# Kernel optimization log

Measured on AMD Instinct MI355X. Metric: run time of the kernel, lower is better.

## Reference

```python
import jax, jax.numpy as jnp
import numpy as np

K = 512
D = 256


def setup_inputs() -> dict:
    key = jax.random.key(0)
    k1, k2 = jax.random.split(key)
    z_e = jax.random.normal(k1, (64, D, 32, 32), dtype=jnp.float32)
    # torch init: uniform_(-1/K, 1/K)
    codebook = jax.random.uniform(k2, (K, D), dtype=jnp.float32, minval=-1.0 / K, maxval=1.0 / K)
    return {"z_e": z_e, "codebook": codebook}


def reference(z_e, codebook):
    B, C, H, W = z_e.shape
    # (B,C,H,W) -> (B,H,W,C) -> (N,D)
    z_flat = jnp.transpose(z_e, (0, 2, 3, 1)).reshape(-1, C)
    # squared L2 distances: ||z||^2 + ||e||^2 - 2 z.e  -> [N, K]
    d = (jnp.sum(z_flat ** 2, axis=1, keepdims=True)
         + jnp.sum(codebook ** 2, axis=1)
         - 2.0 * jnp.matmul(z_flat, codebook.T))
    idx = jnp.argmin(d, axis=1)  # [N]
    z_q_flat = codebook[idx]  # [N, D] gather
    z_q = jnp.transpose(z_q_flat.reshape(B, H, W, C), (0, 3, 1, 2))
    commitment_loss = jnp.mean((z_e - jax.lax.stop_gradient(z_q)) ** 2)
    codebook_loss = jnp.mean((z_q - jax.lax.stop_gradient(z_e)) ** 2)
    # straight-through estimator
    z_q_st = z_e + jax.lax.stop_gradient(z_q - z_e)
    indices = idx.reshape(B, H, W)
    return (z_q_st, commitment_loss, codebook_loss, indices)
```

## Files before the change

### kernel.cpp

```cpp
#include <hip/hip_runtime.h>


typedef __attribute__((ext_vector_type(8))) short short8v;
typedef __attribute__((ext_vector_type(4))) float float4v;
typedef unsigned short ushort_t;

namespace {
constexpr int K = 512;
constexpr int D = 256;
constexpr int HW = 1024;
constexpr int NROWS = 65536;
constexpr int CHW = D * HW;

constexpr int ZQ_SIZE = 64 * CHW;
constexpr int LOSS0_OFF = ZQ_SIZE;
constexpr int LOSS1_OFF = ZQ_SIZE + 1;
constexpr int IDX_OFF = ZQ_SIZE + 2;

constexpr int WS_EH_FLOATS = (K * D) / 2;
constexpr int WS_B = WS_EH_FLOATS;
constexpr int WS_PART = WS_B + K;
constexpr int NBLK = NROWS / 32;

constexpr float EPS_CAND = 2.5e-3f;
}

__device__ __forceinline__ ushort_t bf16_rne(float f) {
    unsigned u = __float_as_uint(f);
    u += 0x7fffu + ((u >> 16) & 1u);
    return (ushort_t)(u >> 16);
}
__device__ __forceinline__ float bf16_to_f(ushort_t h) {
    return __uint_as_float((unsigned)h << 16);
}

__global__ void vq_prep(const float* __restrict__ cb, float* __restrict__ ws) {
    const int k = blockIdx.x;
    const int t = threadIdx.x;
    ushort_t* eh = (ushort_t*)ws;
    eh[(size_t)k * D + t] = bf16_rne(cb[k * D + t]);
    __shared__ float r16[16];
    if (t < 16) {
#pragma clang fp contract(off)
        const float* x = cb + k * D + (t >> 3) * 128;
        const int j = t & 7;
        float v = x[j];
        float r = v * v;
        for (int i = 1; i < 16; ++i) {
            float w = x[8 * i + j];
            r += w * w;
        }
        r16[t] = r;
    }
    __syncthreads();
    if (t == 0) {
#pragma clang fp contract(off)
        float lo = ((r16[0] + r16[1]) + (r16[2] + r16[3])) +
                   ((r16[4] + r16[5]) + (r16[6] + r16[7]));
        float hi = ((r16[8] + r16[9]) + (r16[10] + r16[11])) +
                   ((r16[12] + r16[13]) + (r16[14] + r16[15]));
        ws[WS_B + k] = lo + hi;
    }
}

__global__ __launch_bounds__(256, 2) void vq_mega(
    const float* __restrict__ z_e, const float* __restrict__ cb,
    const ushort_t* __restrict__ eh, const float* __restrict__ Bv,
    float* __restrict__ part, float* __restrict__ out) {
    __shared__ float zf[D][32];
    __shared__ __align__(16) ushort_t zh[32][264];
    __shared__ __align__(16) ushort_t zl[32][264];
    __shared__ float lds_B[K];
    __shared__ float lds_scratch[32][16];
    __shared__ float lds_A[32];
    __shared__ float wmin[4][32];
    __shared__ float rmin[32];
    __shared__ int cnt[32];
    __shared__ float wpart[4];

    const int t = threadIdx.x;
    const int row0 = blockIdx.x * 32;
    const int b = row0 >> 10;
    const int hw0 = row0 & 1023;

    {
        const float4* zb4 = reinterpret_cast<const float4*>(z_e + (size_t)b * CHW + hw0);
        float4* lz4 = reinterpret_cast<float4*>(&zf[0][0]);
        for (int i = t; i < 2048; i += 256) {
            int c = i >> 3, j4 = i & 7;
            lz4[c * 8 + j4] = zb4[c * 256 + j4];
        }
        lds_B[t] = Bv[t];
        lds_B[t + 256] = Bv[t + 256];
    }
    __syncthreads();

    {
#pragma clang fp contract(off)
        const int row = t >> 3;
        const int half = (t >> 2) & 1;
        const int j0 = (t & 3) * 2;
        const int cbase = half * 128;
        float v0 = zf[cbase + j0][row];
        float v1 = zf[cbase + j0 + 1][row];
        float r0 = v0 * v0;
        float r1 = v1 * v1;
        for (int i = 1; i < 16; ++i) {
            float w0 = zf[cbase + 8 * i + j0][row];
            float w1 = zf[cbase + 8 * i + j0 + 1][row];
            r0 += w0 * w0;
            r1 += w1 * w1;
        }
        lds_scratch[row][half * 8 + j0] = r0;
        lds_scratch[row][half * 8 + j0 + 1] = r1;
    }
    {
        const int row = t & 31;
        const int dc = t >> 5;
#pragma unroll
        for (int i = 0; i < 8; ++i) {
            const int d4 = dc * 32 + i * 4;
            ushort_t h[4], l[4];
#pragma unroll
            for (int q = 0; q < 4; ++q) {
                float f = zf[d4 + q][row];
                h[q] = bf16_rne(f);
                l[q] = bf16_rne(f - bf16_to_f(h[q]));
            }
            uint2 ph, pl;
            ph.x = (unsigned)h[0] | ((unsigned)h[1] << 16);
            ph.y = (unsigned)h[2] | ((unsigned)h[3] << 16);
            pl.x = (unsigned)l[0] | ((unsigned)l[1] << 16);
            pl.y = (unsigned)l[2] | ((unsigned)l[3] << 16);
            *reinterpret_cast<uint2*>(&zh[row][d4]) = ph;
            *reinterpret_cast<uint2*>(&zl[row][d4]) = pl;
        }
    }
    __syncthreads();
    if (t < 32) {
#pragma clang fp contract(off)
        const float* r = lds_scratch[t];
        float lo = ((r[0] + r[1]) + (r[2] + r[3])) + ((r[4] + r[5]) + (r[6] + r[7]));
        float hi = ((r[8] + r[9]) + (r[10] + r[11])) + ((r[12] + r[13]) + (r[14] + r[15]));
        lds_A[t] = lo + hi;
    }
    __syncthreads();

    const int lane = t & 63;
    const int w = t >> 6;
    const int wc0 = w * 128;
    const int l15 = lane & 15;
    const int kg = lane >> 4;

    float4v acc[8][2];
#pragma unroll
    for (int c = 0; c < 8; ++c)
#pragma unroll
        for (int rt = 0; rt < 2; ++rt) acc[c][rt] = (float4v)0.f;

    const ushort_t* ehp = eh + (size_t)(wc0 + l15) * D + 8 * kg;

#pragma unroll 4
    for (int d0 = 0; d0 < D; d0 += 32) {
        const short8v bh0 = *reinterpret_cast<const short8v*>(&zh[l15][d0 + 8 * kg]);
        const short8v bh1 = *reinterpret_cast<const short8v*>(&zh[16 + l15][d0 + 8 * kg]);
        const short8v bl0 = *reinterpret_cast<const short8v*>(&zl[l15][d0 + 8 * kg]);
        const short8v bl1 = *reinterpret_cast<const short8v*>(&zl[16 + l15][d0 + 8 * kg]);
#pragma unroll
        for (int c = 0; c < 8; ++c) {
            const short8v a = *reinterpret_cast<const short8v*>(ehp + c * 16 * D + d0);
            acc[c][0] = __builtin_amdgcn_mfma_f32_16x16x32_bf16(a, bh0, acc[c][0], 0, 0, 0);
            acc[c][1] = __builtin_amdgcn_mfma_f32_16x16x32_bf16(a, bh1, acc[c][1], 0, 0, 0);
            acc[c][0] = __builtin_amdgcn_mfma_f32_16x16x32_bf16(a, bl0, acc[c][0], 0, 0, 0);
            acc[c][1] = __builtin_amdgcn_mfma_f32_16x16x32_bf16(a, bl1, acc[c][1], 0, 0, 0);
        }
    }

    float lmin0 = 3.0e38f, lmin1 = 3.0e38f;
#pragma unroll
    for (int c = 0; c < 8; ++c)
#pragma unroll
        for (int rt = 0; rt < 2; ++rt)
#pragma unroll
            for (int r = 0; r < 4; ++r) {
                const int code = wc0 + 16 * c + 4 * kg + r;
                const int row = rt * 16 + l15;
                float s = (lds_A[row] + lds_B[code]) - 2.0f * acc[c][rt][r];
                acc[c][rt][r] = s;
                if (rt == 0) lmin0 = fminf(lmin0, s);
                else lmin1 = fminf(lmin1, s);
            }
    lmin0 = fminf(lmin0, __shfl_xor(lmin0, 16));
    lmin0 = fminf(lmin0, __shfl_xor(lmin0, 32));
    lmin1 = fminf(lmin1, __shfl_xor(lmin1, 16));
    lmin1 = fminf(lmin1, __shfl_xor(lmin1, 32));
    if (lane < 16) {
        wmin[w][l15] = lmin0;
        wmin[w][16 + l15] = lmin1;
    }
    __syncthreads();
    if (t < 32) {
        rmin[t] = fminf(fminf(wmin[0][t], wmin[1][t]), fminf(wmin[2][t], wmin[3][t]));
        cnt[t] = 0;
    }
    __syncthreads();

    int* cand = reinterpret_cast<int*>(&lds_scratch[0][0]);
#pragma unroll
    for (int c = 0; c < 8; ++c)
#pragma unroll
        for (int rt = 0; rt < 2; ++rt) {
            const int row = rt * 16 + l15;
            const float thr = rmin[row] + EPS_CAND;
#pragma unroll
            for (int r = 0; r < 4; ++r) {
                if (acc[c][rt][r] <= thr) {
                    const int code = wc0 + 16 * c + 4 * kg + r;
                    int slot = atomicAdd(&cnt[row], 1);
                    if (slot < 15) cand[row * 15 + slot] = code;
                }
            }
        }
    __syncthreads();

    float* ed = reinterpret_cast<float*>(&zh[0][0]);
    int* ek = reinterpret_cast<int*>(ed + 256);
    int* kb = ek + 256;
    {
        const int row = t & 31;
        const int ct = t >> 5;
        int n = cnt[row];
        if (n > 15) n = 15;
        float bd = 3.0e38f;
        int bk = 0x7fffffff;
        if (n == 1) {
            if (ct == 0) {
                bd = -3.0e38f;
                bk = cand[row * 15];
            }
        } else {
            for (int s = ct; s < n; s += 8) {
                const int k = cand[row * 15 + s];
                const float* ep = cb + (size_t)k * D;
                float a = 0.f;
#pragma unroll 8
                for (int c = 0; c < D; ++c) a = fmaf(zf[c][row], ep[c], a);
                float dv;
                {
#pragma clang fp contract(off)
                    float t1 = lds_A[row] + lds_B[k];
                    dv = t1 - 2.0f * a;
                }
                if (dv < bd || (dv == bd && k < bk)) {
                    bd = dv;
                    bk = k;
                }
            }
        }
        ed[t] = bd;
        ek[t] = bk;
    }
    __syncthreads();
    if (t < 32) {
        float bd = ed[t];
        int bk = ek[t];
#pragma unroll
        for (int q = 1; q < 8; ++q) {
            float od = ed[q * 32 + t];
            int ok = ek[q * 32 + t];
            if (od < bd || (od == bd && ok < bk)) {
                bd = od;
                bk = ok;
            }
        }
        kb[t] = bk;
        out[IDX_OFF + row0 + t] = (float)bk;
    }
    __syncthreads();

    {
        const int j = t & 31;
        const int g = t >> 5;
        const int kme = kb[j];
        const float* ep = cb + (size_t)kme * D;
        float* ob = out + (size_t)b * CHW + hw0;
        float accum = 0.f;
#pragma unroll 4
        for (int i = 0; i < 32; ++i) {
            const int c = g * 32 + i;
            float z = zf[c][j];
            float e = ep[c];
            ob[c * HW + j] = z + (e - z);
            float df = z - e;
            accum = fmaf(df, df, accum);
        }
#pragma unroll
        for (int m = 1; m < 64; m <<= 1) accum += __shfl_xor(accum, m);
        if ((t & 63) == 0) wpart[t >> 6] = accum;
    }
    __syncthreads();
    if (t == 0) part[blockIdx.x] = (wpart[0] + wpart[1]) + (wpart[2] + wpart[3]);
}

__global__ void vq_finish(const float* __restrict__ part, float* __restrict__ out) {
    const int t = threadIdx.x;
    double s = 0.0;
#pragma unroll
    for (int i = 0; i < 8; ++i) s += (double)part[t + 256 * i];
#pragma unroll
    for (int m = 1; m < 64; m <<= 1) s += __shfl_xor(s, m);
    __shared__ double wsum[4];
    if ((t & 63) == 0) wsum[t >> 6] = s;
    __syncthreads();
    if (t == 0) {
        double mean = (wsum[0] + wsum[1] + wsum[2] + wsum[3]) / (double)ZQ_SIZE;
        out[LOSS0_OFF] = (float)mean;
        out[LOSS1_OFF] = (float)mean;
    }
}

extern "C" void kernel_launch(void* const* d_in, const int* in_sizes, int n_in,
                              void* d_out, int out_size, void* d_ws, size_t ws_size,
                              hipStream_t stream) {
    const float* z_e = (const float*)d_in[0];
    const float* cb = (const float*)d_in[1];
    float* out = (float*)d_out;
    float* ws = (float*)d_ws;

    const ushort_t* eh = (const ushort_t*)ws;
    float* Bv = ws + WS_B;
    float* part = ws + WS_PART;

    vq_prep<<<K, D, 0, stream>>>(cb, ws);
    vq_mega<<<NBLK, 256, 0, stream>>>(z_e, cb, eh, Bv, part, out);
    vq_finish<<<1, 256, 0, stream>>>(part, out);
}
```

Baseline: 131.7 us.

## Drop bf16 low-part MFMA pass, free LDS for occupancy, add full-rescan fallback

Removes the split-bf16 (hi+lo) compensation for z, so the distance GEMM uses only the bf16 high part and the MFMA count halves. The fp32 z tile is no longer kept in LDS; z is re-read from global memory for the norms, exact candidate rescoring and the output pass. The LDS saved is used to raise launch bounds to 5 blocks per SM. To keep exactness with the coarser approximation, the candidate epsilon is widened, and a row whose candidate list overflows is rescored exhaustively over all codes. The trade-off is more global/L2 traffic for z and occasional full rescans per row.

Result: slower. 139.9 us (+6.2%).

```diff
diff --git a/kernel.cpp b/kernel.cpp
--- a/kernel.cpp
+++ b/kernel.cpp
@@ -22,16 +22,14 @@
 constexpr int WS_PART = WS_B + K;
 constexpr int NBLK = NROWS / 32;
 
-constexpr float EPS_CAND = 2.5e-3f;
+constexpr float EPS_CAND = 3.0e-3f;
+constexpr int MAXC = 16;
 }
 
 __device__ __forceinline__ ushort_t bf16_rne(float f) {
     unsigned u = __float_as_uint(f);
     u += 0x7fffu + ((u >> 16) & 1u);
     return (ushort_t)(u >> 16);
-}
-__device__ __forceinline__ float bf16_to_f(ushort_t h) {
-    return __uint_as_float((unsigned)h << 16);
 }
 
 __global__ void vq_prep(const float* __restrict__ cb, float* __restrict__ ws) {
@@ -63,15 +61,14 @@
     }
 }
 
-__global__ __launch_bounds__(256, 2) void vq_mega(
+__global__ __launch_bounds__(256, 5) void vq_mega(
     const float* __restrict__ z_e, const float* __restrict__ cb,
     const ushort_t* __restrict__ eh, const float* __restrict__ Bv,
     float* __restrict__ part, float* __restrict__ out) {
-    __shared__ float zf[D][32];
     __shared__ __align__(16) ushort_t zh[32][264];
-    __shared__ __align__(16) ushort_t zl[32][264];
     __shared__ float lds_B[K];
-    __shared__ float lds_scratch[32][16];
+    __shared__ float scr[32][17];
+    __shared__ int cand[32][MAXC];
     __shared__ float lds_A[32];
     __shared__ float wmin[4][32];
     __shared__ float rmin[32];
@@ -82,64 +79,53 @@
     const int row0 = blockIdx.x * 32;
     const int b = row0 >> 10;
     const int hw0 = row0 & 1023;
+    const float* zbase = z_e + (size_t)b * CHW + hw0;
+
+    lds_B[t] = Bv[t];
+    lds_B[t + 256] = Bv[t + 256];
 
     {
-        const float4* zb4 = reinterpret_cast<const float4*>(z_e + (size_t)b * CHW + hw0);
-        float4* lz4 = reinterpret_cast<float4*>(&zf[0][0]);
-        for (int i = t; i < 2048; i += 256) {
-            int c = i >> 3, j4 = i & 7;
-            lz4[c * 8 + j4] = zb4[c * 256 + j4];
-        }
-        lds_B[t] = Bv[t];
-        lds_B[t + 256] = Bv[t + 256];
-    }
-    __syncthreads();
-
-    {
-#pragma clang fp contract(off)
-        const int row = t >> 3;
-        const int half = (t >> 2) & 1;
-        const int j0 = (t & 3) * 2;
-        const int cbase = half * 128;
-        float v0 = zf[cbase + j0][row];
-        float v1 = zf[cbase + j0 + 1][row];
+#pragma clang fp contract(off)
+        const int row = t & 31;
+        const int q = t >> 5;
+        const int half = q >> 2;
+        const int j0 = (q & 3) * 2;
+        const float* zp = zbase + row + (size_t)(half * 128) * HW;
+        float v0 = zp[(size_t)j0 * HW];
+        float v1 = zp[(size_t)(j0 + 1) * HW];
         float r0 = v0 * v0;
         float r1 = v1 * v1;
         for (int i = 1; i < 16; ++i) {
-            float w0 = zf[cbase + 8 * i + j0][row];
-            float w1 = zf[cbase + 8 * i + j0 + 1][row];
+            float w0 = zp[(size_t)(8 * i + j0) * HW];
+            float w1 = zp[(size_t)(8 * i + j0 + 1) * HW];
             r0 += w0 * w0;
             r1 += w1 * w1;
         }
-        lds_scratch[row][half * 8 + j0] = r0;
-        lds_scratch[row][half * 8 + j0 + 1] = r1;
-    }
+        scr[row][half * 8 + j0] = r0;
+        scr[row][half * 8 + j0 + 1] = r1;
+    }
+
     {
         const int row = t & 31;
         const int dc = t >> 5;
+        const float* zp = zbase + row;
 #pragma unroll
         for (int i = 0; i < 8; ++i) {
             const int d4 = dc * 32 + i * 4;
-            ushort_t h[4], l[4];
-#pragma unroll
-            for (int q = 0; q < 4; ++q) {
-                float f = zf[d4 + q][row];
-                h[q] = bf16_rne(f);
-                l[q] = bf16_rne(f - bf16_to_f(h[q]));
-            }
-            uint2 ph, pl;
-            ph.x = (unsigned)h[0] | ((unsigned)h[1] << 16);
-            ph.y = (unsigned)h[2] | ((unsigned)h[3] << 16);
-            pl.x = (unsigned)l[0] | ((unsigned)l[1] << 16);
-            pl.y = (unsigned)l[2] | ((unsigned)l[3] << 16);
+            float f0 = zp[(size_t)(d4 + 0) * HW];
+            float f1 = zp[(size_t)(d4 + 1) * HW];
+            float f2 = zp[(size_t)(d4 + 2) * HW];
+            float f3 = zp[(size_t)(d4 + 3) * HW];
+            uint2 ph;
+            ph.x = (unsigned)bf16_rne(f0) | ((unsigned)bf16_rne(f1) << 16);
+            ph.y = (unsigned)bf16_rne(f2) | ((unsigned)bf16_rne(f3) << 16);
             *reinterpret_cast<uint2*>(&zh[row][d4]) = ph;
-            *reinterpret_cast<uint2*>(&zl[row][d4]) = pl;
         }
     }
     __syncthreads();
     if (t < 32) {
 #pragma clang fp contract(off)
-        const float* r = lds_scratch[t];
+        const float* r = scr[t];
         float lo = ((r[0] + r[1]) + (r[2] + r[3])) + ((r[4] + r[5]) + (r[6] + r[7]));
         float hi = ((r[8] + r[9]) + (r[10] + r[11])) + ((r[12] + r[13]) + (r[14] + r[15]));
         lds_A[t] = lo + hi;
@@ -164,15 +150,11 @@
     for (int d0 = 0; d0 < D; d0 += 32) {
         const short8v bh0 = *reinterpret_cast<const short8v*>(&zh[l15][d0 + 8 * kg]);
         const short8v bh1 = *reinterpret_cast<const short8v*>(&zh[16 + l15][d0 + 8 * kg]);
-        const short8v bl0 = *reinterpret_cast<const short8v*>(&zl[l15][d0 + 8 * kg]);
-        const short8v bl1 = *reinterpret_cast<const short8v*>(&zl[16 + l15][d0 + 8 * kg]);
 #pragma unroll
         for (int c = 0; c < 8; ++c) {
             const short8v a = *reinterpret_cast<const short8v*>(ehp + c * 16 * D + d0);
             acc[c][0] = __builtin_amdgcn_mfma_f32_16x16x32_bf16(a, bh0, acc[c][0], 0, 0, 0);
             acc[c][1] = __builtin_amdgcn_mfma_f32_16x16x32_bf16(a, bh1, acc[c][1], 0, 0, 0);
-            acc[c][0] = __builtin_amdgcn_mfma_f32_16x16x32_bf16(a, bl0, acc[c][0], 0, 0, 0);
-            acc[c][1] = __builtin_amdgcn_mfma_f32_16x16x32_bf16(a, bl1, acc[c][1], 0, 0, 0);
         }
     }
 
@@ -205,7 +187,6 @@
     }
     __syncthreads();
 
-    int* cand = reinterpret_cast<int*>(&lds_scratch[0][0]);
 #pragma unroll
     for (int c = 0; c < 8; ++c)
 #pragma unroll
@@ -217,7 +198,7 @@
                 if (acc[c][rt][r] <= thr) {
                     const int code = wc0 + 16 * c + 4 * kg + r;
                     int slot = atomicAdd(&cnt[row], 1);
-                    if (slot < 15) cand[row * 15 + slot] = code;
+                    if (slot < MAXC) cand[row][slot] = code;
                 }
             }
         }
@@ -229,22 +210,24 @@
     {
         const int row = t & 31;
         const int ct = t >> 5;
-        int n = cnt[row];
-        if (n > 15) n = 15;
+        const float* zp = zbase + row;
+        const int n = cnt[row];
         float bd = 3.0e38f;
         int bk = 0x7fffffff;
         if (n == 1) {
             if (ct == 0) {
                 bd = -3.0e38f;
-                bk = cand[row * 15];
+                bk = cand[row][0];
             }
         } else {
-            for (int s = ct; s < n; s += 8) {
-                const int k = cand[row * 15 + s];
+            const bool full = (n > MAXC);
+            const int lim = full ? K : n;
+            for (int s = ct; s < lim; s += 8) {
+                const int k = full ? s : cand[row][s];
                 const float* ep = cb + (size_t)k * D;
                 float a = 0.f;
 #pragma unroll 8
-                for (int c = 0; c < D; ++c) a = fmaf(zf[c][row], ep[c], a);
+                for (int c = 0; c < D; ++c) a = fmaf(zp[(size_t)c * HW], ep[c], a);
                 float dv;
                 {
 #pragma clang fp contract(off)
@@ -283,14 +266,15 @@
         const int g = t >> 5;
         const int kme = kb[j];
         const float* ep = cb + (size_t)kme * D;
-        float* ob = out + (size_t)b * CHW + hw0;
+        const float* zp = zbase + j;
+        float* ob = out + (size_t)b * CHW + hw0 + j;
         float accum = 0.f;
 #pragma unroll 4
         for (int i = 0; i < 32; ++i) {
             const int c = g * 32 + i;
-            float z = zf[c][j];
+            float z = zp[(size_t)c * HW];
             float e = ep[c];
-            ob[c * HW + j] = z + (e - z);
+            ob[(size_t)c * HW] = z + (e - z);
             float df = z - e;
             accum = fmaf(df, df, accum);
         }
```
